# Kernel optimization log

Hardware: AMD Instinct MI355X
Metric: run time of the kernel (lower is better)

## Reference

```python
import jax, jax.numpy as jnp
import numpy as np

SIGNAL = (32, 32)
KERNEL = (8, 8)
N_FEATURES = [64, 128, 128]
BATCH = 64
ALPHA = 0.5          # source references an undefined global `alpha`; fixed here
LEAKY_SLOPE = 0.01   # torch F.leaky_relu default


def _join_tensor(S, K, loc):
    i = np.arange(S)[:, None, None]
    j = np.arange(S)[None, :, None]
    k = np.arange(K)[None, None, :]
    M = (j >= i) & (i == np.maximum(j, k + loc))
    return jnp.asarray(M.astype(np.float32))


def _meet_tensor(S, K, loc):
    i = np.arange(S)[:, None, None]
    j = np.arange(S)[None, :, None]
    k = np.arange(K)[None, None, :]
    M = (j >= i) & (i == np.minimum(j, k + loc))
    return jnp.asarray(M.astype(np.float32))


def setup_inputs() -> dict:
    key = jax.random.key(0)
    sx, sy = SIGNAL
    kx, ky = KERNEL
    # meet layers use kernel_loc = signal - kernel; join layers use (0, 0)
    cmx = _meet_tensor(sx, kx, sx - kx)
    cmy = _meet_tensor(sy, ky, sy - ky)
    cjx = _join_tensor(sx, kx, 0)
    cjy = _join_tensor(sy, ky, 0)

    keys = jax.random.split(key, 16)
    x = jax.random.normal(keys[0], (BATCH, N_FEATURES[0], sx, sy), dtype=jnp.float32)

    def kaiming(k, shape):
        fan_in = shape[0] * shape[1] * shape[2]  # kx*ky*in_features
        return jax.random.normal(k, shape, dtype=jnp.float32) * np.float32(np.sqrt(2.0 / fan_in))

    inp = {"x": x, "cmx": cmx, "cmy": cmy, "cjx": cjx, "cjy": cjy}
    for li in range(len(N_FEATURES) - 1):
        fi, fo = N_FEATURES[li], N_FEATURES[li + 1]
        inp[f"mw{li}"] = kaiming(keys[1 + 2 * li], (kx, ky, fi, fo))
        inp[f"mb{li}"] = jnp.zeros((fo, 1, 1), dtype=jnp.float32)
        inp[f"jw{li}"] = kaiming(keys[2 + 2 * li], (kx, ky, fi, fo))
        inp[f"jb{li}"] = jnp.zeros((fo, 1, 1), dtype=jnp.float32)
    return inp


def _lattice_conv(cx, cy, X, W, b):
    # Y[m,g,x,y] = sum_{i,j,a,b} cx[i,x,a] cy[j,y,b] X[m,f,i,j] W[a,b,f,g] + bias
    return jnp.einsum('ixa,jyb,mfij,abfg->mgxy', cx, cy, X, W, optimize='optimal') + b


def reference(x, cmx, cmy, cjx, cjy, mw0, mb0, jw0, jb0, mw1, mb1, jw1, jb1):
    params = [(mw0, mb0, jw0, jb0), (mw1, mb1, jw1, jb1)]
    for mw, mb, jw, jb in params:
        m = _lattice_conv(cmx, cmy, x, mw, mb)
        j = _lattice_conv(cjx, cjy, x, jw, jb)
        x = jax.nn.leaky_relu((1.0 - ALPHA) * m + ALPHA * j, negative_slope=LEAKY_SLOPE)
    return x
```

## Files before the change

kernel.cpp:

```cpp
#include <hip/hip_runtime.h>
#include <stdint.h>


typedef __attribute__((ext_vector_type(8))) short short8;
typedef __attribute__((ext_vector_type(4))) float floatx4;
typedef __attribute__((ext_vector_type(4))) unsigned short ushort4v;

__device__ __forceinline__ float bf2f(unsigned short u) {
  union { uint32_t u; float f; } c; c.u = ((uint32_t)u) << 16; return c.f;
}
__device__ __forceinline__ unsigned short f2bf(float f) {
  union { float f; uint32_t u; } c; c.f = f;
  uint32_t u = c.u;
  uint32_t r = (u + 0x7FFFu + ((u >> 16) & 1u)) >> 16;
  return (unsigned short)r;
}

#define SLOT_W1 0
#define SLOT_SB 225
#define SLOT_AS 289
#define SLOT_M  353
#define N_SLOTS 417
#define N_SLOTS_PAD 448

#define NB_SETUP 225
#define NB_PACK 1024
#define NB_TIN 4096
__global__ __launch_bounds__(256) void fused_prep(
    const unsigned short* __restrict__ xa,
    const float* __restrict__ x32,
    const void* __restrict__ mw0, const void* __restrict__ jw0,
    const void* __restrict__ mw1, const void* __restrict__ jw1,
    const void* __restrict__ mb0, const void* __restrict__ jb0,
    const void* __restrict__ mb1, const void* __restrict__ jb1,
    float* __restrict__ bias0, float* __restrict__ bias1,
    int* __restrict__ flag, unsigned short* __restrict__ L,
    unsigned short* __restrict__ PBg0, unsigned short* __restrict__ PBg1,
    unsigned short* __restrict__ Xt0) {
  __shared__ int s_cnt;
  __shared__ unsigned short sh_pack[128][33];
  __shared__ unsigned short sh_tile[32][33];
  int tx = threadIdx.x, ty = threadIdx.y;
  int tid = ty * 32 + tx;
  int bid = blockIdx.x;

  if (bid < NB_SETUP) {
    if (bid == 0) {
      if (tid == 0) s_cnt = 0;
      __syncthreads();
      unsigned short v = xa[tid];
      int e = (v >> 7) & 0xFF;
      int ok = (v == 0) || (e >= 110 && e <= 140);
      atomicAdd(&s_cnt, ok);
      __syncthreads();
      int fp32 = (s_cnt >= 240) ? 0 : 1;
      if (tid == 0) *flag = fp32;
      int g = tid & 127;
      const void* mb = (tid < 128) ? mb0 : mb1;
      const void* jb = (tid < 128) ? jb0 : jb1;
      float* bo = (tid < 128) ? bias0 : bias1;
      float m = fp32 ? ((const float*)mb)[g] : bf2f(((const unsigned short*)mb)[g]);
      float j = fp32 ? ((const float*)jb)[g] : bf2f(((const unsigned short*)jb)[g]);
      bo[g] = 0.5f * (m + j);
      return;
    }
    int t = (bid - 1) * 256 + tid;
    int slot = t >> 7, k = t & 127;
    int isj = k >= 64, ab = k & 63, a = ab >> 3, b = ab & 7;
    float v = 0.f;
    if (slot < 225) {
      int cx = slot / 15, cy = slot % 15;
      int pmx = cx < 7 ? cx : 7, pxx = cx > 7 ? cx - 7 : 0;
      int pmy = cy < 7 ? cy : 7, pyy = cy > 7 ? cy - 7 : 0;
      if (!isj) v = (a >= pxx && b >= pyy) ? 0.5f : 0.f;
      else      v = (a <= pmx && b <= pmy) ? 0.5f : 0.f;
    } else if (slot < 289) {
      int s = slot - SLOT_SB, px = s >> 3, b0 = s & 7;
      if (!isj) v = (a >= px && b == b0) ? 0.5f : 0.f;
    } else if (slot < 353) {
      int s = slot - SLOT_AS, a0 = s >> 3, py = s & 7;
      if (!isj) v = (a == a0 && b >= py) ? 0.5f : 0.f;
    } else if (slot < 417) {
      int s = slot - SLOT_M, a0 = s >> 3, b0 = s & 7;
      if (!isj) v = (a == a0 && b == b0) ? 0.5f : 0.f;
    }
    L[t] = f2bf(v);
    return;
  }

  if (tid == 0) s_cnt = 0;
  __syncthreads();
  {
    unsigned short v = xa[tid];
    int e = (v >> 7) & 0xFF;
    int ok = (v == 0) || (e >= 110 && e <= 140);
    atomicAdd(&s_cnt, ok);
  }
  __syncthreads();
  int fp32 = (s_cnt >= 240) ? 0 : 1;

  if (bid < NB_SETUP + NB_PACK) {
    int pb = bid - NB_SETUP;
    int gx = pb & 3, gy = (pb >> 2) & 127, layer = pb >> 9;
    int F = layer ? 128 : 64;
    int f = gy;
    if (f >= F) return;
    int g0 = gx * 32;
    const int G = 128, FG = F * G;
    const void* mw = layer ? mw1 : mw0;
    const void* jw = layer ? jw1 : jw0;
    unsigned short* PB = layer ? PBg1 : PBg0;
    for (int k = ty; k < 128; k += 8) {
      const void* src = (k < 64) ? mw : jw;
      int ab = k & 63;
      size_t idx = (size_t)ab * FG + (size_t)f * G + g0 + tx;
      sh_pack[k][tx] = fp32 ? f2bf(((const float*)src)[idx])
                            : ((const unsigned short*)src)[idx];
    }
    __syncthreads();
    int kk = tid & 127, gs = tid >> 7;
    for (int gg = gs; gg < 32; gg += 2)
      PB[((size_t)(g0 + gg) * F + f) * 128 + kk] = sh_pack[kk][gg];
    return;
  }

  {
    int tbi = bid - (NB_SETUP + NB_PACK);
    const int R = 4096, C = 1024;
    int c0 = (tbi & 31) * 32, r0 = (tbi >> 5) * 32;
    int row = tid >> 3, vc = tid & 7;
    if (fp32) {
      floatx4 lv = *(const floatx4*)&x32[(size_t)(r0 + row) * C + c0 + vc * 4];
#pragma unroll
      for (int j = 0; j < 4; ++j) sh_tile[row][vc * 4 + j] = f2bf(lv[j]);
    } else {
      ushort4v lv = *(const ushort4v*)&xa[(size_t)(r0 + row) * C + c0 + vc * 4];
#pragma unroll
      for (int j = 0; j < 4; ++j) sh_tile[row][vc * 4 + j] = lv[j];
    }
    __syncthreads();
    ushort4v w;
#pragma unroll
    for (int j = 0; j < 4; ++j) w[j] = sh_tile[vc * 4 + j][row];
    *(ushort4v*)&Xt0[(size_t)(c0 + row) * R + r0 + vc * 4] = w;
  }
}

__global__ __launch_bounds__(256) void transpose_out(
    const unsigned short* __restrict__ src, unsigned short* __restrict__ d16,
    float* __restrict__ d32, int R, int C, const int* __restrict__ flag) {
  __shared__ unsigned short tile[32][33];
  int fp32 = *flag;
  int tx = threadIdx.x, ty = threadIdx.y;
  int c0 = blockIdx.x * 32, r0 = blockIdx.y * 32;
  ushort4v v = *(const ushort4v*)&src[(size_t)(r0 + ty) * C + c0 + tx * 4];
#pragma unroll
  for (int j = 0; j < 4; ++j) tile[ty][tx * 4 + j] = v[j];
  __syncthreads();
  if (fp32) {
    floatx4 w;
#pragma unroll
    for (int j = 0; j < 4; ++j) w[j] = bf2f(tile[tx * 4 + j][ty]);
    *(floatx4*)&d32[(size_t)(c0 + ty) * R + r0 + tx * 4] = w;
  } else {
    ushort4v w;
#pragma unroll
    for (int j = 0; j < 4; ++j) w[j] = tile[tx * 4 + j][ty];
    *(ushort4v*)&d16[(size_t)(c0 + ty) * R + r0 + tx * 4] = w;
  }
}

template <int F, int NT>
__device__ __forceinline__ void mfma_tile(
    const unsigned short* __restrict__ A, const unsigned short* __restrict__ W,
    floatx4 acc[NT], int wave, int n, int q) {
  const unsigned short* a_ptr = A + ((size_t)(wave * 16 + n)) * F + q * 8;
  const unsigned short* w_ptr = W + (size_t)n * F + q * 8;
#pragma unroll
  for (int kk = 0; kk < F; kk += 32) {
    short8 av = *(const short8*)(a_ptr + kk);
#pragma unroll
    for (int t = 0; t < NT; ++t) {
      short8 bv = *(const short8*)(w_ptr + (size_t)t * 16 * F + kk);
      acc[t] = __builtin_amdgcn_mfma_f32_16x16x32_bf16(av, bv, acc[t], 0, 0, 0);
    }
  }
}

__global__ __launch_bounds__(256) void prep_gemm2(
    const unsigned short* __restrict__ L,
    const unsigned short* __restrict__ PBg0,
    const unsigned short* __restrict__ PBg1,
    unsigned short* __restrict__ Wall0, unsigned short* __restrict__ Wall1) {
  int layer = blockIdx.z;
  int GF = layer ? 16384 : 8192;
  int n0 = blockIdx.x * 128;
  if (n0 >= GF) return;
  int m0 = blockIdx.y * 64;
  const unsigned short* PB = layer ? PBg1 : PBg0;
  unsigned short* Wall = layer ? Wall1 : Wall0;
  int wave = threadIdx.x >> 6, lane = threadIdx.x & 63;
  int n = lane & 15, q = lane >> 4;
  floatx4 acc[8];
#pragma unroll
  for (int t = 0; t < 8; ++t) acc[t] = (floatx4){0.f, 0.f, 0.f, 0.f};
  mfma_tile<128, 8>(L + (size_t)m0 * 128, PB + (size_t)n0 * 128, acc, wave, n, q);
#pragma unroll
  for (int t = 0; t < 8; ++t) {
    int gcol = n0 + t * 16 + n;
#pragma unroll
    for (int r = 0; r < 4; ++r) {
      int m = m0 + wave * 16 + q * 4 + r;
      Wall[(size_t)m * GF + gcol] = f2bf(acc[t][r]);
    }
  }
}

template <int F>
__global__ __launch_bounds__(256) void corr_gemm(
    const unsigned short* __restrict__ Xt, const unsigned short* __restrict__ Wall,
    unsigned short* __restrict__ V, unsigned short* __restrict__ U,
    unsigned short* __restrict__ T) {
  int bid = blockIdx.x, gsh = blockIdx.y;
  int wave = threadIdx.x >> 6, lane = threadIdx.x & 63;
  int n = lane & 15, q = lane >> 4;
  floatx4 acc[4];
#pragma unroll
  for (int t = 0; t < 4; ++t) acc[t] = (floatx4){0.f, 0.f, 0.f, 0.f};
  for (int i = 0; i < 8; ++i) {
    int ipos, slot;
    unsigned short* out;
    if (bid < 32) {
      int y = bid, a = i;
      int py = y > 24 ? y - 24 : 0;
      ipos = (24 + a) * 32 + y;
      slot = SLOT_AS + a * 8 + py;
      out = V + (size_t)(a * 32 + y) * 8192;
    } else if (bid < 64) {
      int x = bid - 32, b = i;
      int px = x > 24 ? x - 24 : 0;
      ipos = x * 32 + 24 + b;
      slot = SLOT_SB + px * 8 + b;
      out = U + (size_t)(b * 32 + x) * 8192;
    } else {
      int a = bid - 64, b = i;
      ipos = (24 + a) * 32 + 24 + b;
      slot = SLOT_M + a * 8 + b;
      out = T + (size_t)(a * 8 + b) * 8192;
    }
    mfma_tile<F, 4>(Xt + (size_t)ipos * 64 * F,
                    Wall + ((size_t)slot * 128 + gsh * 64) * F, acc, wave, n, q);
#pragma unroll
    for (int t = 0; t < 4; ++t) {
      int gcol = gsh * 64 + t * 16 + n;
#pragma unroll
      for (int r = 0; r < 4; ++r) {
        int m = wave * 16 + q * 4 + r;
        out[(size_t)m * 128 + gcol] = f2bf(acc[t][r]);
      }
    }
  }
}

template <int F>
__global__ __launch_bounds__(256) void final_gemm(
    const unsigned short* __restrict__ Xt, const unsigned short* __restrict__ Wall,
    const unsigned short* __restrict__ V, const unsigned short* __restrict__ U,
    const unsigned short* __restrict__ T, const float* __restrict__ bias,
    unsigned short* __restrict__ Out) {
  int pos = blockIdx.x;
  int x = pos >> 5, y = pos & 31;
  int wave = threadIdx.x >> 6, lane = threadIdx.x & 63;
  int n = lane & 15, q = lane >> 4;
  int clsx = x < 7 ? x : (x <= 24 ? 7 : x - 17);
  int clsy = y < 7 ? y : (y <= 24 ? 7 : y - 17);
  int px = x > 24 ? x - 24 : 0;
  int py = y > 24 ? y - 24 : 0;
  const unsigned short* c3 = px ? V + ((size_t)(px - 1) * 32 + y) * 8192 : nullptr;
  const unsigned short* c2 = py ? U + ((size_t)(py - 1) * 32 + x) * 8192 : nullptr;

  floatx4 acc[8];
#pragma unroll
  for (int t = 0; t < 8; ++t) {
    int gcol = t * 16 + n;
    float bv = bias[gcol];
#pragma unroll
    for (int r = 0; r < 4; ++r) {
      int m = wave * 16 + q * 4 + r;
      size_t idx = (size_t)m * 128 + gcol;
      float v = bv;
      if (c3) v += bf2f(c3[idx]);
      if (c2) v += bf2f(c2[idx]);
      acc[t][r] = v;
    }
  }
  if (px && py) {
    const unsigned short* c4b = T + (size_t)(py - 1) * 8192;
    for (int a2 = 0; a2 < px; ++a2) {
#pragma unroll
      for (int t = 0; t < 8; ++t) {
        int gcol = t * 16 + n;
#pragma unroll
        for (int r = 0; r < 4; ++r) {
          int m = wave * 16 + q * 4 + r;
          acc[t][r] += bf2f(c4b[(size_t)a2 * 65536 + (size_t)m * 128 + gcol]);
        }
      }
    }
  }

  mfma_tile<F, 8>(Xt + (size_t)pos * 64 * F,
                  Wall + (size_t)(SLOT_W1 + clsx * 15 + clsy) * 128 * F,
                  acc, wave, n, q);

  unsigned short* o = Out + (size_t)pos * 64 * 128;
#pragma unroll
  for (int t = 0; t < 8; ++t) {
    int gcol = t * 16 + n;
#pragma unroll
    for (int r = 0; r < 4; ++r) {
      int m = wave * 16 + q * 4 + r;
      float v = acc[t][r];
      v = v > 0.f ? v : 0.01f * v;
      o[(size_t)m * 128 + gcol] = f2bf(v);
    }
  }
}

extern "C" void kernel_launch(void* const* d_in, const int* in_sizes, int n_in,
                              void* d_out, int out_size, void* d_ws,
                              size_t ws_size, hipStream_t stream) {
  const void* x   = d_in[0];
  const void* mw0 = d_in[5];
  const void* mb0 = d_in[6];
  const void* jw0 = d_in[7];
  const void* jb0 = d_in[8];
  const void* mw1 = d_in[9];
  const void* mb1 = d_in[10];
  const void* jw1 = d_in[11];
  const void* jb1 = d_in[12];

  char* ws = (char*)d_ws;
  const size_t MB = 1u << 20;
  unsigned short* Xt0   = (unsigned short*)(ws + 0);
  unsigned short* A1    = (unsigned short*)(ws + 9 * MB);
  unsigned short* Wall0 = (unsigned short*)(ws + 26 * MB);
  unsigned short* Wall1 = (unsigned short*)(ws + 34 * MB);
  unsigned short* Out2  = (unsigned short*)(ws + 49 * MB);
  unsigned short* PBg0  = (unsigned short*)(ws + 66 * MB);
  unsigned short* PBg1  = (unsigned short*)(ws + 69 * MB);
  unsigned short* L     = (unsigned short*)(ws + 74 * MB);
  float* bias0 = (float*)(ws + 75 * MB);
  float* bias1 = bias0 + 128;
  int*   flag  = (int*)(bias1 + 128);
  unsigned short* V = (unsigned short*)(ws + 76 * MB);
  unsigned short* U = (unsigned short*)(ws + 81 * MB);
  unsigned short* T = (unsigned short*)(ws + 86 * MB);

  dim3 tb(32, 8);
  fused_prep<<<NB_SETUP + NB_PACK + NB_TIN, tb, 0, stream>>>(
      (const unsigned short*)x, (const float*)x, mw0, jw0, mw1, jw1,
      mb0, jb0, mb1, jb1, bias0, bias1, flag, L, PBg0, PBg1, Xt0);
  prep_gemm2<<<dim3(128, 7, 2), 256, 0, stream>>>(L, PBg0, PBg1, Wall0, Wall1);

  corr_gemm<64><<<dim3(72, 2), 256, 0, stream>>>(Xt0, Wall0, V, U, T);
  final_gemm<64><<<dim3(1024), 256, 0, stream>>>(Xt0, Wall0, V, U, T,
                                                 bias0, A1);
  corr_gemm<128><<<dim3(72, 2), 256, 0, stream>>>(A1, Wall1, V, U, T);
  final_gemm<128><<<dim3(1024), 256, 0, stream>>>(A1, Wall1, V, U, T,
                                                  bias1, Out2);

  transpose_out<<<dim3(256, 32), dim3(8, 32), 0, stream>>>(
      Out2, (unsigned short*)d_out, (float*)d_out, 1024, 8192, flag);
}
```

Baseline: 255.2 us.

## Split GEMM output columns across more blocks and transpose correction buffers

The correction GEMM now uses four column shards of 32 instead of two of 64, and the final GEMM adds a second grid dimension so each block computes 64 output columns instead of 128. This doubles the block count and cuts per-thread accumulator registers. The V/U/T correction buffers move to a column-major layout, so writes and reads become 4-wide vector accesses instead of scattered scalar ones. The final GEMM also inlines the MFMA loop with the A fragments preloaded into registers. In exchange, each A tile is loaded by twice as many blocks.

```diff
diff --git a/kernel.cpp b/kernel.cpp
--- a/kernel.cpp
+++ b/kernel.cpp
@@ -224,9 +224,10 @@
   int bid = blockIdx.x, gsh = blockIdx.y;
   int wave = threadIdx.x >> 6, lane = threadIdx.x & 63;
   int n = lane & 15, q = lane >> 4;
-  floatx4 acc[4];
-#pragma unroll
-  for (int t = 0; t < 4; ++t) acc[t] = (floatx4){0.f, 0.f, 0.f, 0.f};
+  int m0 = wave * 16 + q * 4;
+  floatx4 acc[2];
+#pragma unroll
+  for (int t = 0; t < 2; ++t) acc[t] = (floatx4){0.f, 0.f, 0.f, 0.f};
   for (int i = 0; i < 8; ++i) {
     int ipos, slot;
     unsigned short* out;
@@ -248,16 +249,15 @@
       slot = SLOT_M + a * 8 + b;
       out = T + (size_t)(a * 8 + b) * 8192;
     }
-    mfma_tile<F, 4>(Xt + (size_t)ipos * 64 * F,
-                    Wall + ((size_t)slot * 128 + gsh * 64) * F, acc, wave, n, q);
-#pragma unroll
-    for (int t = 0; t < 4; ++t) {
-      int gcol = gsh * 64 + t * 16 + n;
-#pragma unroll
-      for (int r = 0; r < 4; ++r) {
-        int m = wave * 16 + q * 4 + r;
-        out[(size_t)m * 128 + gcol] = f2bf(acc[t][r]);
-      }
+    mfma_tile<F, 2>(Xt + (size_t)ipos * 64 * F,
+                    Wall + ((size_t)slot * 128 + gsh * 32) * F, acc, wave, n, q);
+#pragma unroll
+    for (int t = 0; t < 2; ++t) {
+      int gcol = gsh * 32 + t * 16 + n;
+      ushort4v w;
+#pragma unroll
+      for (int r = 0; r < 4; ++r) w[r] = f2bf(acc[t][r]);
+      *(ushort4v*)&out[(size_t)gcol * 64 + m0] = w;
     }
   }
 }
@@ -268,58 +268,80 @@
     const unsigned short* __restrict__ V, const unsigned short* __restrict__ U,
     const unsigned short* __restrict__ T, const float* __restrict__ bias,
     unsigned short* __restrict__ Out) {
-  int pos = blockIdx.x;
+  int pos = blockIdx.x, gs = blockIdx.y;
   int x = pos >> 5, y = pos & 31;
   int wave = threadIdx.x >> 6, lane = threadIdx.x & 63;
   int n = lane & 15, q = lane >> 4;
+  int m0 = wave * 16 + q * 4;
   int clsx = x < 7 ? x : (x <= 24 ? 7 : x - 17);
   int clsy = y < 7 ? y : (y <= 24 ? 7 : y - 17);
   int px = x > 24 ? x - 24 : 0;
   int py = y > 24 ? y - 24 : 0;
-  const unsigned short* c3 = px ? V + ((size_t)(px - 1) * 32 + y) * 8192 : nullptr;
-  const unsigned short* c2 = py ? U + ((size_t)(py - 1) * 32 + x) * 8192 : nullptr;
-
-  floatx4 acc[8];
-#pragma unroll
-  for (int t = 0; t < 8; ++t) {
-    int gcol = t * 16 + n;
-    float bv = bias[gcol];
-#pragma unroll
-    for (int r = 0; r < 4; ++r) {
-      int m = wave * 16 + q * 4 + r;
-      size_t idx = (size_t)m * 128 + gcol;
-      float v = bv;
-      if (c3) v += bf2f(c3[idx]);
-      if (c2) v += bf2f(c2[idx]);
-      acc[t][r] = v;
+
+  const unsigned short* a_ptr =
+      Xt + (size_t)pos * 64 * F + ((size_t)(wave * 16 + n)) * F + q * 8;
+  short8 av[F / 32];
+#pragma unroll
+  for (int kk = 0; kk < F / 32; ++kk)
+    av[kk] = *(const short8*)(a_ptr + kk * 32);
+
+  floatx4 acc[4];
+#pragma unroll
+  for (int t = 0; t < 4; ++t) {
+    float bv = bias[gs * 64 + t * 16 + n];
+#pragma unroll
+    for (int r = 0; r < 4; ++r) acc[t][r] = bv;
+  }
+  if (px) {
+    const unsigned short* c3 = V + ((size_t)(px - 1) * 32 + y) * 8192;
+#pragma unroll
+    for (int t = 0; t < 4; ++t) {
+      ushort4v v = *(const ushort4v*)&c3[(size_t)(gs * 64 + t * 16 + n) * 64 + m0];
+#pragma unroll
+      for (int r = 0; r < 4; ++r) acc[t][r] += bf2f(v[r]);
+    }
+  }
+  if (py) {
+    const unsigned short* c2 = U + ((size_t)(py - 1) * 32 + x) * 8192;
+#pragma unroll
+    for (int t = 0; t < 4; ++t) {
+      ushort4v v = *(const ushort4v*)&c2[(size_t)(gs * 64 + t * 16 + n) * 64 + m0];
+#pragma unroll
+      for (int r = 0; r < 4; ++r) acc[t][r] += bf2f(v[r]);
     }
   }
   if (px && py) {
     const unsigned short* c4b = T + (size_t)(py - 1) * 8192;
     for (int a2 = 0; a2 < px; ++a2) {
 #pragma unroll
-      for (int t = 0; t < 8; ++t) {
-        int gcol = t * 16 + n;
-#pragma unroll
-        for (int r = 0; r < 4; ++r) {
-          int m = wave * 16 + q * 4 + r;
-          acc[t][r] += bf2f(c4b[(size_t)a2 * 65536 + (size_t)m * 128 + gcol]);
-        }
+      for (int t = 0; t < 4; ++t) {
+        ushort4v v = *(const ushort4v*)&c4b[(size_t)a2 * 65536 +
+                                            (size_t)(gs * 64 + t * 16 + n) * 64 + m0];
+#pragma unroll
+        for (int r = 0; r < 4; ++r) acc[t][r] += bf2f(v[r]);
       }
     }
   }
 
-  mfma_tile<F, 8>(Xt + (size_t)pos * 64 * F,
-                  Wall + (size_t)(SLOT_W1 + clsx * 15 + clsy) * 128 * F,
-                  acc, wave, n, q);
+  const unsigned short* w_ptr =
+      Wall + ((size_t)(SLOT_W1 + clsx * 15 + clsy) * 128 + gs * 64) * F +
+      (size_t)n * F + q * 8;
+#pragma unroll
+  for (int kk = 0; kk < F / 32; ++kk) {
+#pragma unroll
+    for (int t = 0; t < 4; ++t) {
+      short8 bv = *(const short8*)(w_ptr + (size_t)t * 16 * F + kk * 32);
+      acc[t] = __builtin_amdgcn_mfma_f32_16x16x32_bf16(av[kk], bv, acc[t], 0, 0, 0);
+    }
+  }
 
   unsigned short* o = Out + (size_t)pos * 64 * 128;
 #pragma unroll
-  for (int t = 0; t < 8; ++t) {
-    int gcol = t * 16 + n;
+  for (int t = 0; t < 4; ++t) {
+    int gcol = gs * 64 + t * 16 + n;
 #pragma unroll
     for (int r = 0; r < 4; ++r) {
-      int m = wave * 16 + q * 4 + r;
+      int m = m0 + r;
       float v = acc[t][r];
       v = v > 0.f ? v : 0.01f * v;
       o[(size_t)m * 128 + gcol] = f2bf(v);
@@ -363,12 +385,12 @@
       mb0, jb0, mb1, jb1, bias0, bias1, flag, L, PBg0, PBg1, Xt0);
   prep_gemm2<<<dim3(128, 7, 2), 256, 0, stream>>>(L, PBg0, PBg1, Wall0, Wall1);
 
-  corr_gemm<64><<<dim3(72, 2), 256, 0, stream>>>(Xt0, Wall0, V, U, T);
-  final_gemm<64><<<dim3(1024), 256, 0, stream>>>(Xt0, Wall0, V, U, T,
-                                                 bias0, A1);
-  corr_gemm<128><<<dim3(72, 2), 256, 0, stream>>>(A1, Wall1, V, U, T);
-  final_gemm<128><<<dim3(1024), 256, 0, stream>>>(A1, Wall1, V, U, T,
-                                                  bias1, Out2);
+  corr_gemm<64><<<dim3(72, 4), 256, 0, stream>>>(Xt0, Wall0, V, U, T);
+  final_gemm<64><<<dim3(1024, 2), 256, 0, stream>>>(Xt0, Wall0, V, U, T,
+                                                    bias0, A1);
+  corr_gemm<128><<<dim3(72, 4), 256, 0, stream>>>(A1, Wall1, V, U, T);
+  final_gemm<128><<<dim3(1024, 2), 256, 0, stream>>>(A1, Wall1, V, U, T,
+                                                     bias1, Out2);
 
   transpose_out<<<dim3(256, 32), dim3(8, 32), 0, stream>>>(
       Out2, (unsigned short*)d_out, (float*)d_out, 1024, 8192, flag);
```

New measurement: 244.7 us (median of 2 runs). 4.1% less time.
